# Kernel tuning notes

Measured on AMD Instinct MI355X. Metric: run time of the kernel, lower is better.

Reference implementation:

```python
import jax, jax.numpy as jnp
import numpy as np

B, S, D, H = 2, 2048, 1024, 16
DK = D // H


def setup_inputs() -> dict:
    key = jax.random.key(0)
    ks = jax.random.split(key, 11)
    sd = 1.0 / np.sqrt(D)  # torch Linear default init scale (uniform bound)
    def lin(k):
        kw, kb = jax.random.split(k)
        W = jax.random.uniform(kw, (D, D), jnp.float32, -sd, sd)
        b = jax.random.uniform(kb, (D,), jnp.float32, -sd, sd)
        return W, b
    Wq, bq = lin(ks[0]); Wk, bk = lin(ks[1]); Wv, bv = lin(ks[2]); Wo, bo = lin(ks[3])
    return {
        "Q": jax.random.normal(ks[4], (B, S, D), jnp.float32),
        "K": jax.random.normal(ks[5], (B, S, D), jnp.float32),
        "V": jax.random.normal(ks[6], (B, S, D), jnp.float32),
        "mask": jnp.ones((B, S), jnp.int32),
        "Wq": Wq, "bq": bq, "Wk": Wk, "bk": bk,
        "Wv": Wv, "bv": bv, "Wo": Wo, "bo": bo,
    }


def reference(Q, K, V, mask, Wq, bq, Wk, bk, Wv, bv, Wo, bo):
    b, s, _ = Q.shape
    # projections (torch Linear: x @ W.T + b), split heads -> [b, h, s, dk]
    def proj(x, W, bias):
        return (x @ W.T + bias).reshape(b, -1, H, DK).transpose(0, 2, 1, 3)
    q = proj(Q, Wq, bq)
    k = proj(K, Wk, bk)
    v = proj(V, Wv, bv)
    scores = jnp.einsum('bhqd,bhkd->bhqk', q, k) / jnp.sqrt(jnp.float32(DK))
    m = mask[:, None, None, :]  # [b,1,1,s_k]
    scores = jnp.where(m == 0, jnp.float32(-jnp.inf), scores)
    attn = jax.nn.softmax(scores, axis=-1)
    out = jnp.einsum('bhqk,bhkd->bhqd', attn, v)
    out = out.transpose(0, 2, 1, 3).reshape(b, s, H * DK)
    return out @ Wo.T + bo
```

## Files before the change

kernel.cpp:

```cpp
#include <hip/hip_runtime.h>
#include <stdint.h>

#define BB 2
#define HH 16
#define SS 2048
#define DKK 64
#define DD 1024
#define TT (BB * SS)

typedef __attribute__((ext_vector_type(8))) short bf16x8;
typedef __attribute__((ext_vector_type(4))) float f32x4;
typedef __attribute__((ext_vector_type(16))) float f32x16;

static __device__ __forceinline__ unsigned short f2bf(float f) {
  union { float f; uint32_t u; } c; c.f = f;
  return (unsigned short)((c.u + 0x7FFFu + ((c.u >> 16) & 1u)) >> 16);
}

static __device__ __forceinline__ f32x4 zero4() {
  f32x4 z; z[0] = 0.f; z[1] = 0.f; z[2] = 0.f; z[3] = 0.f; return z;
}
static __device__ __forceinline__ f32x16 zero16() {
  f32x16 z;
#pragma unroll
  for (int i = 0; i < 16; ++i) z[i] = 0.f;
  return z;
}

static __device__ __forceinline__ uint32_t cvt_pk_bf16(float lo, float hi) {
  uint32_t r;
  asm("v_cvt_pk_bf16_f32 %0, %1, %2" : "=v"(r) : "v"(lo), "v"(hi));
  return r;
}

static __device__ __forceinline__ float max3f(float a, float b, float c) {
  float r;
  asm("v_max3_f32 %0, %1, %2, %3" : "=v"(r) : "v"(a), "v"(b), "v"(c));
  return r;
}

static __device__ __forceinline__ uint32_t xswap_u32(uint32_t v) {
  return (uint32_t)__shfl_xor((int)v, 32);
}
static __device__ __forceinline__ float xhalf_max(float x) {
  return fmaxf(x, __shfl_xor(x, 32));
}
static __device__ __forceinline__ float xhalf_sum(float x) {
  return x + __shfl_xor(x, 32);
}

static __device__ __forceinline__ void gload_lds16(const void* g, void* l) {
  __builtin_amdgcn_global_load_lds(
      (const __attribute__((address_space(1))) void*)g,
      (__attribute__((address_space(3))) void*)l, 16, 0, 0);
}

static __device__ __forceinline__ int swz(int row, int col) {
  return ((((col >> 3) ^ row) & 7) << 3) | (col & 7);
}

struct CvtArgs {
  const float* src[7];
  unsigned short* dst[7];
  int n4[7];
};

__global__ __launch_bounds__(256) void cvt_all(CvtArgs a) {
  const int id = blockIdx.y;
  const float4* s = (const float4*)a.src[id];
  ushort4* d = (ushort4*)a.dst[id];
  const int n4 = a.n4[id];
  for (int i = blockIdx.x * blockDim.x + threadIdx.x; i < n4;
       i += gridDim.x * blockDim.x) {
    float4 v = s[i];
    ushort4 o;
    o.x = f2bf(v.x); o.y = f2bf(v.y); o.z = f2bf(v.z); o.w = f2bf(v.w);
    d[i] = o;
  }
}

struct GemmJob {
  const unsigned short* A;
  const unsigned short* W;
  const float* bias;
  void* out;
  int mode;
  float scale;
};
struct GemmArgs { GemmJob job[3]; };

template <int BM>
__global__ __launch_bounds__(256) void gemm_kernel(GemmArgs args) {
  constexpr int MI = BM / 32;
  __shared__ __align__(16) unsigned short As[BM][64];
  __shared__ __align__(16) unsigned short Bs[128][64];
  const GemmJob jb = args.job[blockIdx.z];
  const int tid = threadIdx.x;
  const int lane = tid & 63;
  const int wv = tid >> 6;
  const int fr = lane & 15, fq = lane >> 4;
  const int wr = (wv >> 1) * (BM / 2), wc = (wv & 1) * 64;
  const int m0 = blockIdx.y * BM, n0 = blockIdx.x * 128;
  const int lrow = lane >> 3;
  const int lchunk = (lane & 7) ^ lrow;
  const unsigned short* __restrict__ A = jb.A;
  const unsigned short* __restrict__ W = jb.W;

  f32x4 acc[MI][4];
#pragma unroll
  for (int i = 0; i < MI; ++i)
#pragma unroll
    for (int j = 0; j < 4; ++j) acc[i][j] = zero4();

  constexpr int SEGA_W = BM / 32;

  for (int k0 = 0; k0 < DD; k0 += 64) {
    __syncthreads();
#pragma unroll
    for (int i = 0; i < SEGA_W; ++i) {
      const int seg = wv * SEGA_W + i;
      const int row = seg * 8 + lrow;
      gload_lds16(A + (size_t)(m0 + row) * DD + k0 + lchunk * 8,
                  (char*)&As[0][0] + seg * 1024);
    }
#pragma unroll
    for (int i = 0; i < 4; ++i) {
      const int seg = wv * 4 + i;
      const int row = seg * 8 + lrow;
      gload_lds16(W + (size_t)(n0 + row) * DD + k0 + lchunk * 8,
                  (char*)&Bs[0][0] + seg * 1024);
    }
    __syncthreads();
#pragma unroll
    for (int kk = 0; kk < 2; ++kk) {
      bf16x8 af[MI], bfr[4];
#pragma unroll
      for (int i = 0; i < MI; ++i) {
        const int r = wr + i * 16 + fr;
        af[i] = *(const bf16x8*)&As[r][swz(r, kk * 32 + fq * 8)];
      }
#pragma unroll
      for (int j = 0; j < 4; ++j) {
        const int r = wc + j * 16 + fr;
        bfr[j] = *(const bf16x8*)&Bs[r][swz(r, kk * 32 + fq * 8)];
      }
      __builtin_amdgcn_s_setprio(1);
#pragma unroll
      for (int i = 0; i < MI; ++i)
#pragma unroll
        for (int j = 0; j < 4; ++j)
          acc[i][j] = __builtin_amdgcn_mfma_f32_16x16x32_bf16(af[i], bfr[j],
                                                              acc[i][j], 0, 0, 0);
      __builtin_amdgcn_s_setprio(0);
    }
  }

  const int mode = jb.mode;
  const float scale = jb.scale;
  if (mode == 1) {
    float* out = (float*)jb.out;
#pragma unroll
    for (int i = 0; i < MI; ++i)
#pragma unroll
      for (int j = 0; j < 4; ++j) {
        const int col = n0 + wc + j * 16 + fr;
        const float bv = jb.bias[col];
#pragma unroll
        for (int r = 0; r < 4; ++r) {
          const int row = m0 + wr + i * 16 + fq * 4 + r;
          out[(size_t)row * DD + col] = (acc[i][j][r] + bv) * scale;
        }
      }
  } else if (mode == 0) {
    unsigned short* out = (unsigned short*)jb.out;
#pragma unroll
    for (int i = 0; i < MI; ++i)
#pragma unroll
      for (int j = 0; j < 4; ++j) {
        const int col = n0 + wc + j * 16 + fr;
        const float bv = jb.bias[col];
        const int h = col >> 6, dk = col & 63;
#pragma unroll
        for (int r = 0; r < 4; ++r) {
          const int row = m0 + wr + i * 16 + fq * 4 + r;
          const int b = row >> 11, s = row & (SS - 1);
          out[(((size_t)(b * HH + h)) * SS + s) * DKK + dk] =
              f2bf((acc[i][j][r] + bv) * scale);
        }
      }
  } else {
    unsigned short* out = (unsigned short*)jb.out;
#pragma unroll
    for (int i = 0; i < MI; ++i)
#pragma unroll
      for (int j = 0; j < 4; ++j) {
        const int col = n0 + wc + j * 16 + fr;
        const float bv = jb.bias[col];
        const int h = col >> 6, dk = col & 63;
#pragma unroll
        for (int r = 0; r < 4; ++r) {
          const int row = m0 + wr + i * 16 + fq * 4 + r;
          const int b = row >> 11, s = row & (SS - 1);
          out[(((size_t)(b * HH + h)) * DKK + dk) * SS + s] =
              f2bf((acc[i][j][r] + bv) * scale);
        }
      }
  }
}

__global__ __launch_bounds__(256) void attn_kernel(
    const unsigned short* __restrict__ qh, const unsigned short* __restrict__ kh,
    const unsigned short* __restrict__ vt, const int* __restrict__ maskp,
    unsigned short* __restrict__ ao) {
  __shared__ __align__(16) unsigned short Ks[2][64][64];
  __shared__ __align__(16) unsigned short Vts[2][64][64];

  const int tid = threadIdx.x;
  const int lane = tid & 63, wv = tid >> 6;
  const int lo = lane & 31, hi = lane >> 5;

  int bid = blockIdx.x;
  const int virt = (bid & 7) * 64 + (bid >> 3);
  const int bh = virt >> 4, qblk = virt & 15;
  const int bB = bh >> 4, h = bh & 15;
  const int q0 = qblk * 128;
  const size_t base = (size_t)bh * SS * DKK;
  const size_t vbase = (size_t)bh * DKK * SS;

  bf16x8 aq[4];
  {
    const int qrow = q0 + wv * 32 + lo;
#pragma unroll
    for (int t = 0; t < 4; ++t)
      aq[t] = *(const bf16x8*)(qh + base + (size_t)qrow * DKK + 16 * t + hi * 8);
  }

  float mrun = -1e30f, lsum = 0.f;
  f32x16 o0 = zero16(), o1 = zero16();

  const int r0 = tid >> 3, cc0 = tid & 7;
  const int r1 = (tid + 256) >> 3, cc1 = tid & 7;

  bf16x8 rk[2], rv[2];
#define LOADT(kv0)                                                            \
  {                                                                           \
    rk[0] = *(const bf16x8*)(kh + base + (size_t)((kv0) + r0) * DKK + cc0*8); \
    rk[1] = *(const bf16x8*)(kh + base + (size_t)((kv0) + r1) * DKK + cc1*8); \
    rv[0] = *(const bf16x8*)(vt + vbase + (size_t)r0 * SS + (kv0) + cc0*8);   \
    rv[1] = *(const bf16x8*)(vt + vbase + (size_t)r1 * SS + (kv0) + cc1*8);   \
  }
#define STORET(buf)                                                           \
  {                                                                           \
    *(bf16x8*)&Ks[buf][r0][swz(r0, cc0 * 8)] = rk[0];                         \
    *(bf16x8*)&Ks[buf][r1][swz(r1, cc1 * 8)] = rk[1];                         \
    *(bf16x8*)&Vts[buf][r0][swz(r0, cc0 * 8)] = rv[0];                        \
    *(bf16x8*)&Vts[buf][r1][swz(r1, cc1 * 8)] = rv[1];                        \
  }

  LOADT(0);
  STORET(0);
  LOADT(64);
  int mcur = maskp[bB * SS + lane];
  int mnxt = maskp[bB * SS + 64 + lane];

  int cur = 0;
  constexpr int NT = SS / 64;

  for (int t = 0; t < NT; ++t) {
    __syncthreads();
    if (t + 1 < NT) {
      STORET(cur ^ 1);
      if (t + 2 < NT) LOADT((t + 2) * 64);
    }

    const int mt = mcur;
    const bool allones = __all(mt != 0);

    f32x16 s0 = zero16(), s1 = zero16();
    __builtin_amdgcn_s_setprio(1);
#pragma unroll
    for (int tt = 0; tt < 4; ++tt) {
      bf16x8 k0 = *(const bf16x8*)&Ks[cur][lo][swz(lo, (hi + 2 * tt) * 8)];
      bf16x8 k1 = *(const bf16x8*)&Ks[cur][32 + lo][swz(32 + lo, (hi + 2 * tt) * 8)];
      s0 = __builtin_amdgcn_mfma_f32_32x32x16_bf16(k0, aq[tt], s0, 0, 0, 0);
      s1 = __builtin_amdgcn_mfma_f32_32x32x16_bf16(k1, aq[tt], s1, 0, 0, 0);
    }
    __builtin_amdgcn_s_setprio(0);

    if (!allones) {
#pragma unroll
      for (int r = 0; r < 16; ++r) {
        const int kvb = (r & 3) + 8 * (r >> 2) + 4 * hi;
        s0[r] += (__shfl(mt, kvb) != 0) ? 0.f : -1e30f;
        s1[r] += (__shfl(mt, 32 + kvb) != 0) ? 0.f : -1e30f;
      }
    }

    float tm = fmaxf(s0[0], s1[0]);
#pragma unroll
    for (int r = 1; r < 16; ++r) tm = max3f(tm, s0[r], s1[r]);
    tm = xhalf_max(tm);

    if (__any(tm - mrun > 8.f)) {
      const float mnew = fmaxf(mrun, tm);
      const float scl = __builtin_amdgcn_exp2f(mrun - mnew);
      lsum *= scl;
#pragma unroll
      for (int r = 0; r < 16; ++r) { o0[r] *= scl; o1[r] *= scl; }
      mrun = mnew;
    }

    float ps = 0.f;
#pragma unroll
    for (int r = 0; r < 16; ++r) {
      s0[r] = __builtin_amdgcn_exp2f(s0[r] - mrun);
      s1[r] = __builtin_amdgcn_exp2f(s1[r] - mrun);
      ps += s0[r] + s1[r];
    }
    lsum += xhalf_sum(ps);

    bf16x8 pb[4];
#pragma unroll
    for (int kb = 0; kb < 2; ++kb) {
      const f32x16& s = kb ? s1 : s0;
#pragma unroll
      for (int tt = 0; tt < 2; ++tt) {
        const int b = tt * 8;
        uint32_t a0 = cvt_pk_bf16(s[b + 0], s[b + 1]);
        uint32_t a1 = cvt_pk_bf16(s[b + 2], s[b + 3]);
        uint32_t a2 = cvt_pk_bf16(s[b + 4], s[b + 5]);
        uint32_t a3 = cvt_pk_bf16(s[b + 6], s[b + 7]);
        const uint32_t e0 = xswap_u32(hi ? a0 : a2);
        const uint32_t e1 = xswap_u32(hi ? a1 : a3);
        union { uint32_t w[4]; bf16x8 v; } u;
        u.w[0] = hi ? e0 : a0;
        u.w[1] = hi ? e1 : a1;
        u.w[2] = hi ? a2 : e0;
        u.w[3] = hi ? a3 : e1;
        pb[kb * 2 + tt] = u.v;
      }
    }

    __builtin_amdgcn_s_setprio(1);
#pragma unroll
    for (int tt = 0; tt < 4; ++tt) {
      bf16x8 v0 = *(const bf16x8*)&Vts[cur][lo][swz(lo, (hi + 2 * tt) * 8)];
      bf16x8 v1 = *(const bf16x8*)&Vts[cur][32 + lo][swz(32 + lo, (hi + 2 * tt) * 8)];
      o0 = __builtin_amdgcn_mfma_f32_32x32x16_bf16(v0, pb[tt], o0, 0, 0, 0);
      o1 = __builtin_amdgcn_mfma_f32_32x32x16_bf16(v1, pb[tt], o1, 0, 0, 0);
    }
    __builtin_amdgcn_s_setprio(0);

    mcur = mnxt;
    if (t + 2 < NT) mnxt = maskp[bB * SS + (t + 2) * 64 + lane];
    cur ^= 1;
  }

  const float inv = 1.f / lsum;
  const int token = bB * SS + q0 + wv * 32 + lo;
  unsigned short* aop = ao + (size_t)token * DD + h * DKK;
#pragma unroll
  for (int jb = 0; jb < 2; ++jb) {
    const f32x16& o = jb ? o1 : o0;
#pragma unroll
    for (int g = 0; g < 4; ++g) {
      uint2 w;
      w.x = cvt_pk_bf16(o[4 * g + 0] * inv, o[4 * g + 1] * inv);
      w.y = cvt_pk_bf16(o[4 * g + 2] * inv, o[4 * g + 3] * inv);
      *(uint2*)&aop[jb * 32 + 8 * g + 4 * hi] = w;
    }
  }
#undef LOADT
#undef STORET
}

extern "C" void kernel_launch(void* const* d_in, const int* in_sizes, int n_in,
                              void* d_out, int out_size, void* d_ws, size_t ws_size,
                              hipStream_t stream) {
  const float* Q = (const float*)d_in[0];
  const float* K = (const float*)d_in[1];
  const float* V = (const float*)d_in[2];
  const int* mask = (const int*)d_in[3];
  const float* Wq = (const float*)d_in[4];
  const float* bq = (const float*)d_in[5];
  const float* Wk = (const float*)d_in[6];
  const float* bk = (const float*)d_in[7];
  const float* Wv = (const float*)d_in[8];
  const float* bv = (const float*)d_in[9];
  const float* Wo = (const float*)d_in[10];
  const float* bo = (const float*)d_in[11];

  char* ws = (char*)d_ws;
  const size_t SZ_X = (size_t)TT * DD * 2;
  const size_t SZ_W = (size_t)DD * DD * 2;
  unsigned short* Qb = (unsigned short*)(ws + 0 * SZ_X);
  unsigned short* Kb = (unsigned short*)(ws + 1 * SZ_X);
  unsigned short* Vb = (unsigned short*)(ws + 2 * SZ_X);
  unsigned short* Wqb = (unsigned short*)(ws + 3 * SZ_X);
  unsigned short* Wkb = (unsigned short*)(ws + 3 * SZ_X + 1 * SZ_W);
  unsigned short* Wvb = (unsigned short*)(ws + 3 * SZ_X + 2 * SZ_W);
  unsigned short* Wob = (unsigned short*)(ws + 3 * SZ_X + 3 * SZ_W);
  unsigned short* qh = (unsigned short*)(ws + 3 * SZ_X + 4 * SZ_W);
  unsigned short* kh = (unsigned short*)(ws + 4 * SZ_X + 4 * SZ_W);
  unsigned short* vt = (unsigned short*)(ws + 5 * SZ_X + 4 * SZ_W);
  unsigned short* ao = (unsigned short*)(ws + 6 * SZ_X + 4 * SZ_W);

  CvtArgs ca;
  ca.src[0] = Q;  ca.dst[0] = Qb;  ca.n4[0] = TT * DD / 4;
  ca.src[1] = K;  ca.dst[1] = Kb;  ca.n4[1] = TT * DD / 4;
  ca.src[2] = V;  ca.dst[2] = Vb;  ca.n4[2] = TT * DD / 4;
  ca.src[3] = Wq; ca.dst[3] = Wqb; ca.n4[3] = DD * DD / 4;
  ca.src[4] = Wk; ca.dst[4] = Wkb; ca.n4[4] = DD * DD / 4;
  ca.src[5] = Wv; ca.dst[5] = Wvb; ca.n4[5] = DD * DD / 4;
  ca.src[6] = Wo; ca.dst[6] = Wob; ca.n4[6] = DD * DD / 4;
  cvt_all<<<dim3(1024, 7), 256, 0, stream>>>(ca);

  const float SCALE_Q = 0.125f * 1.44269504088896f;

  GemmArgs ga;
  ga.job[0] = {Qb, Wqb, bq, qh, 0, SCALE_Q};
  ga.job[1] = {Kb, Wkb, bk, kh, 0, 1.0f};
  ga.job[2] = {Vb, Wvb, bv, vt, 2, 1.0f};
  gemm_kernel<128><<<dim3(DD / 128, TT / 128, 3), 256, 0, stream>>>(ga);

  attn_kernel<<<dim3((TT / 128) * HH), 256, 0, stream>>>(qh, kh, vt, mask, ao);

  GemmArgs gf;
  gf.job[0] = {ao, Wob, bo, d_out, 1, 1.0f};
  gf.job[1] = gf.job[0];
  gf.job[2] = gf.job[0];
  gemm_kernel<64><<<dim3(DD / 128, TT / 64, 1), 256, 0, stream>>>(gf);
}
```

Baseline: 138.8 us.

## Split KV range across two wave groups with direct-to-LDS loads and merge

The attention kernel now uses 512-thread blocks covering 256 query rows, with two wave groups each processing half of the KV sequence (split-K flash attention) and combining partial softmax state through LDS at the end. Each wave handles two 32-row query subtiles so every K/V LDS fragment feeds twice as many MFMAs. K/V tiles are staged with direct global-to-LDS loads instead of register round-trips. The cost is a 64KB LDS footprint, higher register pressure from doubled accumulators, and an extra merge/synchronisation epilogue.

```diff
diff --git a/kernel.cpp b/kernel.cpp
--- a/kernel.cpp
+++ b/kernel.cpp
@@ -208,170 +208,226 @@
   }
 }
 
-__global__ __launch_bounds__(256) void attn_kernel(
+__global__ __launch_bounds__(512, 2) void attn_kernel(
     const unsigned short* __restrict__ qh, const unsigned short* __restrict__ kh,
     const unsigned short* __restrict__ vt, const int* __restrict__ maskp,
     unsigned short* __restrict__ ao) {
-  __shared__ __align__(16) unsigned short Ks[2][64][64];
-  __shared__ __align__(16) unsigned short Vts[2][64][64];
+  __shared__ __align__(16) char smem[65536];
 
   const int tid = threadIdx.x;
   const int lane = tid & 63, wv = tid >> 6;
   const int lo = lane & 31, hi = lane >> 5;
-
-  int bid = blockIdx.x;
-  const int virt = (bid & 7) * 64 + (bid >> 3);
-  const int bh = virt >> 4, qblk = virt & 15;
+  const int g = wv >> 2, qw = wv & 3;
+
+  const int bid = blockIdx.x;
+  const int virt = (bid & 7) * 32 + (bid >> 3);
+  const int bh = virt >> 3, qblk = virt & 7;
   const int bB = bh >> 4, h = bh & 15;
-  const int q0 = qblk * 128;
+  const int q0 = qblk * 256;
   const size_t base = (size_t)bh * SS * DKK;
   const size_t vbase = (size_t)bh * DKK * SS;
 
-  bf16x8 aq[4];
-  {
-    const int qrow = q0 + wv * 32 + lo;
-#pragma unroll
-    for (int t = 0; t < 4; ++t)
-      aq[t] = *(const bf16x8*)(qh + base + (size_t)qrow * DKK + 16 * t + hi * 8);
-  }
-
-  float mrun = -1e30f, lsum = 0.f;
-  f32x16 o0 = zero16(), o1 = zero16();
-
-  const int r0 = tid >> 3, cc0 = tid & 7;
-  const int r1 = (tid + 256) >> 3, cc1 = tid & 7;
-
-  bf16x8 rk[2], rv[2];
-#define LOADT(kv0)                                                            \
+  const int lrow = lane >> 3;
+  const int lchunk = (lane & 7) ^ lrow;
+  const int srow = wv * 8 + lrow;
+
+  bf16x8 aq[2][4];
+#pragma unroll
+  for (int st = 0; st < 2; ++st) {
+    const int qrow = q0 + qw * 64 + st * 32 + lo;
+#pragma unroll
+    for (int tt = 0; tt < 4; ++tt)
+      aq[st][tt] =
+          *(const bf16x8*)(qh + base + (size_t)qrow * DKK + 16 * tt + hi * 8);
+  }
+
+  float mrun[2] = {-1e30f, -1e30f}, lsum[2] = {0.f, 0.f};
+  f32x16 o[2][2];
+#pragma unroll
+  for (int st = 0; st < 2; ++st) {
+    o[st][0] = zero16();
+    o[st][1] = zero16();
+  }
+
+  const int kvb = g * (SS / 2);
+
+#define STAGE(d, t)                                                           \
   {                                                                           \
-    rk[0] = *(const bf16x8*)(kh + base + (size_t)((kv0) + r0) * DKK + cc0*8); \
-    rk[1] = *(const bf16x8*)(kh + base + (size_t)((kv0) + r1) * DKK + cc1*8); \
-    rv[0] = *(const bf16x8*)(vt + vbase + (size_t)r0 * SS + (kv0) + cc0*8);   \
-    rv[1] = *(const bf16x8*)(vt + vbase + (size_t)r1 * SS + (kv0) + cc1*8);   \
-  }
-#define STORET(buf)                                                           \
-  {                                                                           \
-    *(bf16x8*)&Ks[buf][r0][swz(r0, cc0 * 8)] = rk[0];                         \
-    *(bf16x8*)&Ks[buf][r1][swz(r1, cc1 * 8)] = rk[1];                         \
-    *(bf16x8*)&Vts[buf][r0][swz(r0, cc0 * 8)] = rv[0];                        \
-    *(bf16x8*)&Vts[buf][r1][swz(r1, cc1 * 8)] = rv[1];                        \
-  }
-
-  LOADT(0);
-  STORET(0);
-  LOADT(64);
-  int mcur = maskp[bB * SS + lane];
-  int mnxt = maskp[bB * SS + 64 + lane];
-
+    const int ka = (t) * 64, kb2 = SS / 2 + (t) * 64;                         \
+    gload_lds16(kh + base + (size_t)(ka + srow) * DKK + lchunk * 8,           \
+                smem + ((d)) * 8192 + wv * 1024);                             \
+    gload_lds16(vt + vbase + (size_t)srow * SS + ka + lchunk * 8,             \
+                smem + 32768 + ((d)) * 8192 + wv * 1024);                     \
+    gload_lds16(kh + base + (size_t)(kb2 + srow) * DKK + lchunk * 8,          \
+                smem + (2 + (d)) * 8192 + wv * 1024);                         \
+    gload_lds16(vt + vbase + (size_t)srow * SS + kb2 + lchunk * 8,            \
+                smem + 32768 + (2 + (d)) * 8192 + wv * 1024);                 \
+  }
+
+  STAGE(0, 0);
   int cur = 0;
-  constexpr int NT = SS / 64;
-
-  for (int t = 0; t < NT; ++t) {
+  constexpr int NTH = SS / 128;
+
+  for (int t = 0; t < NTH; ++t) {
     __syncthreads();
-    if (t + 1 < NT) {
-      STORET(cur ^ 1);
-      if (t + 2 < NT) LOADT((t + 2) * 64);
-    }
-
-    const int mt = mcur;
+    if (t + 1 < NTH) STAGE(cur ^ 1, t + 1);
+    const int mt = maskp[bB * SS + kvb + t * 64 + lane];
+
+    const unsigned short* Ksb =
+        (const unsigned short*)(smem + (g * 2 + cur) * 8192);
+    const unsigned short* Vsb =
+        (const unsigned short*)(smem + 32768 + (g * 2 + cur) * 8192);
+
+    f32x16 sc[2][2];
+#pragma unroll
+    for (int st = 0; st < 2; ++st) { sc[st][0] = zero16(); sc[st][1] = zero16(); }
+    __builtin_amdgcn_s_setprio(1);
+#pragma unroll
+    for (int tt = 0; tt < 4; ++tt) {
+      bf16x8 k0 = *(const bf16x8*)&Ksb[lo * 64 + swz(lo, (hi + 2 * tt) * 8)];
+      bf16x8 k1 =
+          *(const bf16x8*)&Ksb[(32 + lo) * 64 + swz(32 + lo, (hi + 2 * tt) * 8)];
+#pragma unroll
+      for (int st = 0; st < 2; ++st) {
+        sc[st][0] =
+            __builtin_amdgcn_mfma_f32_32x32x16_bf16(k0, aq[st][tt], sc[st][0], 0, 0, 0);
+        sc[st][1] =
+            __builtin_amdgcn_mfma_f32_32x32x16_bf16(k1, aq[st][tt], sc[st][1], 0, 0, 0);
+      }
+    }
+    __builtin_amdgcn_s_setprio(0);
+
     const bool allones = __all(mt != 0);
-
-    f32x16 s0 = zero16(), s1 = zero16();
+    if (!allones) {
+#pragma unroll
+      for (int r = 0; r < 16; ++r) {
+        const int kvi = (r & 3) + 8 * (r >> 2) + 4 * hi;
+        const float a0 = (__shfl(mt, kvi) != 0) ? 0.f : -1e30f;
+        const float a1 = (__shfl(mt, 32 + kvi) != 0) ? 0.f : -1e30f;
+#pragma unroll
+        for (int st = 0; st < 2; ++st) {
+          sc[st][0][r] += a0;
+          sc[st][1][r] += a1;
+        }
+      }
+    }
+
+    bf16x8 pb[2][4];
+#pragma unroll
+    for (int st = 0; st < 2; ++st) {
+      float pm[8];
+#pragma unroll
+      for (int i = 0; i < 8; ++i)
+        pm[i] = fmaxf(fmaxf(sc[st][0][2 * i], sc[st][0][2 * i + 1]),
+                      fmaxf(sc[st][1][2 * i], sc[st][1][2 * i + 1]));
+      float tm = fmaxf(max3f(pm[0], pm[1], pm[2]), max3f(pm[3], pm[4], pm[5]));
+      tm = max3f(tm, pm[6], pm[7]);
+      tm = xhalf_max(tm);
+
+      if (__any(tm - mrun[st] > 8.f)) {
+        const float mnew = fmaxf(mrun[st], tm);
+        const float scl = __builtin_amdgcn_exp2f(mrun[st] - mnew);
+        lsum[st] *= scl;
+#pragma unroll
+        for (int r = 0; r < 16; ++r) {
+          o[st][0][r] *= scl;
+          o[st][1][r] *= scl;
+        }
+        mrun[st] = mnew;
+      }
+
+#pragma unroll
+      for (int r = 0; r < 16; ++r) {
+        sc[st][0][r] = __builtin_amdgcn_exp2f(sc[st][0][r] - mrun[st]);
+        sc[st][1][r] = __builtin_amdgcn_exp2f(sc[st][1][r] - mrun[st]);
+      }
+      float t8[8];
+#pragma unroll
+      for (int i = 0; i < 8; ++i)
+        t8[i] = (sc[st][0][2 * i] + sc[st][0][2 * i + 1]) +
+                (sc[st][1][2 * i] + sc[st][1][2 * i + 1]);
+      const float ps =
+          ((t8[0] + t8[1]) + (t8[2] + t8[3])) + ((t8[4] + t8[5]) + (t8[6] + t8[7]));
+      lsum[st] += xhalf_sum(ps);
+
+#pragma unroll
+      for (int kb = 0; kb < 2; ++kb) {
+#pragma unroll
+        for (int tt = 0; tt < 2; ++tt) {
+          const int b = tt * 8;
+          uint32_t a0 = cvt_pk_bf16(sc[st][kb][b + 0], sc[st][kb][b + 1]);
+          uint32_t a1 = cvt_pk_bf16(sc[st][kb][b + 2], sc[st][kb][b + 3]);
+          uint32_t a2 = cvt_pk_bf16(sc[st][kb][b + 4], sc[st][kb][b + 5]);
+          uint32_t a3 = cvt_pk_bf16(sc[st][kb][b + 6], sc[st][kb][b + 7]);
+          const uint32_t e0 = xswap_u32(hi ? a0 : a2);
+          const uint32_t e1 = xswap_u32(hi ? a1 : a3);
+          union { uint32_t w[4]; bf16x8 v; } u;
+          u.w[0] = hi ? e0 : a0;
+          u.w[1] = hi ? e1 : a1;
+          u.w[2] = hi ? a2 : e0;
+          u.w[3] = hi ? a3 : e1;
+          pb[st][kb * 2 + tt] = u.v;
+        }
+      }
+    }
+
     __builtin_amdgcn_s_setprio(1);
 #pragma unroll
     for (int tt = 0; tt < 4; ++tt) {
-      bf16x8 k0 = *(const bf16x8*)&Ks[cur][lo][swz(lo, (hi + 2 * tt) * 8)];
-      bf16x8 k1 = *(const bf16x8*)&Ks[cur][32 + lo][swz(32 + lo, (hi + 2 * tt) * 8)];
-      s0 = __builtin_amdgcn_mfma_f32_32x32x16_bf16(k0, aq[tt], s0, 0, 0, 0);
-      s1 = __builtin_amdgcn_mfma_f32_32x32x16_bf16(k1, aq[tt], s1, 0, 0, 0);
+      bf16x8 v0 = *(const bf16x8*)&Vsb[lo * 64 + swz(lo, (hi + 2 * tt) * 8)];
+      bf16x8 v1 =
+          *(const bf16x8*)&Vsb[(32 + lo) * 64 + swz(32 + lo, (hi + 2 * tt) * 8)];
+#pragma unroll
+      for (int st = 0; st < 2; ++st) {
+        o[st][0] = __builtin_amdgcn_mfma_f32_32x32x16_bf16(v0, pb[st][tt], o[st][0], 0, 0, 0);
+        o[st][1] = __builtin_amdgcn_mfma_f32_32x32x16_bf16(v1, pb[st][tt], o[st][1], 0, 0, 0);
+      }
     }
     __builtin_amdgcn_s_setprio(0);
 
-    if (!allones) {
-#pragma unroll
-      for (int r = 0; r < 16; ++r) {
-        const int kvb = (r & 3) + 8 * (r >> 2) + 4 * hi;
-        s0[r] += (__shfl(mt, kvb) != 0) ? 0.f : -1e30f;
-        s1[r] += (__shfl(mt, 32 + kvb) != 0) ? 0.f : -1e30f;
-      }
-    }
-
-    float tm = fmaxf(s0[0], s1[0]);
-#pragma unroll
-    for (int r = 1; r < 16; ++r) tm = max3f(tm, s0[r], s1[r]);
-    tm = xhalf_max(tm);
-
-    if (__any(tm - mrun > 8.f)) {
-      const float mnew = fmaxf(mrun, tm);
-      const float scl = __builtin_amdgcn_exp2f(mrun - mnew);
-      lsum *= scl;
-#pragma unroll
-      for (int r = 0; r < 16; ++r) { o0[r] *= scl; o1[r] *= scl; }
-      mrun = mnew;
-    }
-
-    float ps = 0.f;
-#pragma unroll
-    for (int r = 0; r < 16; ++r) {
-      s0[r] = __builtin_amdgcn_exp2f(s0[r] - mrun);
-      s1[r] = __builtin_amdgcn_exp2f(s1[r] - mrun);
-      ps += s0[r] + s1[r];
-    }
-    lsum += xhalf_sum(ps);
-
-    bf16x8 pb[4];
-#pragma unroll
-    for (int kb = 0; kb < 2; ++kb) {
-      const f32x16& s = kb ? s1 : s0;
-#pragma unroll
-      for (int tt = 0; tt < 2; ++tt) {
-        const int b = tt * 8;
-        uint32_t a0 = cvt_pk_bf16(s[b + 0], s[b + 1]);
-        uint32_t a1 = cvt_pk_bf16(s[b + 2], s[b + 3]);
-        uint32_t a2 = cvt_pk_bf16(s[b + 4], s[b + 5]);
-        uint32_t a3 = cvt_pk_bf16(s[b + 6], s[b + 7]);
-        const uint32_t e0 = xswap_u32(hi ? a0 : a2);
-        const uint32_t e1 = xswap_u32(hi ? a1 : a3);
-        union { uint32_t w[4]; bf16x8 v; } u;
-        u.w[0] = hi ? e0 : a0;
-        u.w[1] = hi ? e1 : a1;
-        u.w[2] = hi ? a2 : e0;
-        u.w[3] = hi ? a3 : e1;
-        pb[kb * 2 + tt] = u.v;
-      }
-    }
-
-    __builtin_amdgcn_s_setprio(1);
-#pragma unroll
-    for (int tt = 0; tt < 4; ++tt) {
-      bf16x8 v0 = *(const bf16x8*)&Vts[cur][lo][swz(lo, (hi + 2 * tt) * 8)];
-      bf16x8 v1 = *(const bf16x8*)&Vts[cur][32 + lo][swz(32 + lo, (hi + 2 * tt) * 8)];
-      o0 = __builtin_amdgcn_mfma_f32_32x32x16_bf16(v0, pb[tt], o0, 0, 0, 0);
-      o1 = __builtin_amdgcn_mfma_f32_32x32x16_bf16(v1, pb[tt], o1, 0, 0, 0);
-    }
-    __builtin_amdgcn_s_setprio(0);
-
-    mcur = mnxt;
-    if (t + 2 < NT) mnxt = maskp[bB * SS + (t + 2) * 64 + lane];
     cur ^= 1;
   }
-
-  const float inv = 1.f / lsum;
-  const int token = bB * SS + q0 + wv * 32 + lo;
-  unsigned short* aop = ao + (size_t)token * DD + h * DKK;
-#pragma unroll
-  for (int jb = 0; jb < 2; ++jb) {
-    const f32x16& o = jb ? o1 : o0;
-#pragma unroll
-    for (int g = 0; g < 4; ++g) {
-      uint2 w;
-      w.x = cvt_pk_bf16(o[4 * g + 0] * inv, o[4 * g + 1] * inv);
-      w.y = cvt_pk_bf16(o[4 * g + 2] * inv, o[4 * g + 3] * inv);
-      *(uint2*)&aop[jb * 32 + 8 * g + 4 * hi] = w;
-    }
-  }
-#undef LOADT
-#undef STORET
+#undef STAGE
+
+  float* mb = (float*)smem;
+#pragma unroll
+  for (int st = 0; st < 2; ++st) {
+    const int rec = (qw * 64 + lane) * 34;
+    __syncthreads();
+    if (g == 1) {
+      mb[rec] = mrun[st];
+      mb[rec + 1] = lsum[st];
+#pragma unroll
+      for (int i = 0; i < 16; ++i) {
+        mb[rec + 2 + i] = o[st][0][i];
+        mb[rec + 18 + i] = o[st][1][i];
+      }
+    }
+    __syncthreads();
+    if (g == 0) {
+      const float m1 = mb[rec], l1 = mb[rec + 1];
+      const float ms = fmaxf(mrun[st], m1);
+      const float a = __builtin_amdgcn_exp2f(mrun[st] - ms);
+      const float b = __builtin_amdgcn_exp2f(m1 - ms);
+      const float inv = 1.f / (lsum[st] * a + l1 * b);
+      const int token = bB * SS + q0 + qw * 64 + st * 32 + lo;
+      unsigned short* aop = ao + (size_t)token * DD + h * DKK;
+#pragma unroll
+      for (int db = 0; db < 2; ++db) {
+#pragma unroll
+        for (int gq = 0; gq < 4; ++gq) {
+          float c0 = (o[st][db][4 * gq + 0] * a + mb[rec + 2 + db * 16 + 4 * gq + 0] * b) * inv;
+          float c1 = (o[st][db][4 * gq + 1] * a + mb[rec + 2 + db * 16 + 4 * gq + 1] * b) * inv;
+          float c2 = (o[st][db][4 * gq + 2] * a + mb[rec + 2 + db * 16 + 4 * gq + 2] * b) * inv;
+          float c3 = (o[st][db][4 * gq + 3] * a + mb[rec + 2 + db * 16 + 4 * gq + 3] * b) * inv;
+          uint2 w;
+          w.x = cvt_pk_bf16(c0, c1);
+          w.y = cvt_pk_bf16(c2, c3);
+          *(uint2*)&aop[db * 32 + 8 * gq + 4 * hi] = w;
+        }
+      }
+    }
+  }
 }
 
 extern "C" void kernel_launch(void* const* d_in, const int* in_sizes, int n_in,
@@ -423,7 +479,7 @@
   ga.job[2] = {Vb, Wvb, bv, vt, 2, 1.0f};
   gemm_kernel<128><<<dim3(DD / 128, TT / 128, 3), 256, 0, stream>>>(ga);
 
-  attn_kernel<<<dim3((TT / 128) * HH), 256, 0, stream>>>(qh, kh, vt, mask, ao);
+  attn_kernel<<<dim3((TT / 256) * HH), 512, 0, stream>>>(qh, kh, vt, mask, ao);
 
   GemmArgs gf;
   gf.job[0] = {ao, Wob, bo, d_out, 1, 1.0f};
```

New measurement: 132.5 us. 4.5% less time.
